# Kernel tuning notes

Measured on AMD Instinct MI355X. Metric: run time of the kernel, lower is better.

Reference implementation:

```python
import jax, jax.numpy as jnp
import numpy as np

WS = 7           # window_size
NUM_HEADS = 4
DIM = 128
BNW = 4096       # batch * num_windows
NW = 64          # windows per image (attn_mask leading dim)
N = WS * WS      # tokens per window = 49


def make_rel_idx(ws: int) -> np.ndarray:
    coords = np.stack(np.meshgrid(np.arange(ws), np.arange(ws), indexing='ij'))  # (2, ws, ws)
    flat = coords.reshape(2, -1)                                                  # (2, N)
    rel = flat[:, :, None] - flat[:, None, :]                                     # (2, N, N)
    rel = rel.transpose(1, 2, 0).copy()
    rel[:, :, 0] += ws - 1
    rel[:, :, 1] += ws - 1
    rel[:, :, 0] *= 2 * ws - 1
    return rel.sum(-1).astype(np.int32)                                           # (N, N)


def setup_inputs() -> dict:
    key = jax.random.key(0)
    ks = jax.random.split(key, 4)
    x = jax.random.normal(ks[0], (BNW, N, DIM), dtype=jnp.float32)
    attn_mask = jnp.zeros((NW, N, N), dtype=jnp.float32)
    qkv_w = jax.random.normal(ks[1], (3 * DIM, DIM), dtype=jnp.float32) * 0.02
    qkv_b = jnp.zeros((3 * DIM,), dtype=jnp.float32)
    proj_w = jax.random.normal(ks[2], (DIM, DIM), dtype=jnp.float32) * 0.02
    proj_b = jnp.zeros((DIM,), dtype=jnp.float32)
    bias_table = jax.random.normal(ks[3], ((2 * WS - 1) ** 2, NUM_HEADS), dtype=jnp.float32) * 0.02
    rel_idx = jnp.asarray(make_rel_idx(WS))
    return {"x": x, "attn_mask": attn_mask, "qkv_w": qkv_w, "qkv_b": qkv_b,
            "proj_w": proj_w, "proj_b": proj_b, "bias_table": bias_table,
            "rel_idx": rel_idx}


def reference(x, attn_mask, qkv_w, qkv_b, proj_w, proj_b, bias_table, rel_idx):
    BnW, n, C = x.shape
    H = NUM_HEADS
    hd = C // H
    scale = hd ** -0.5
    # qkv projection: (BnW, n, 3C) -> (3, BnW, H, n, hd)
    qkv = (x @ qkv_w.T + qkv_b).reshape(BnW, n, 3, H, hd).transpose(2, 0, 3, 1, 4)
    q, k, v = qkv[0], qkv[1], qkv[2]
    attn = jnp.einsum('bhnd,bhmd->bhnm', q * scale, k)          # (BnW, H, n, n)
    bias = bias_table[rel_idx]                                   # (n, n, H)
    attn = attn + bias.transpose(2, 0, 1)[None]                  # broadcast (1, H, n, n)
    nW = attn_mask.shape[0]
    attn = attn.reshape(-1, nW, H, n, n) + attn_mask[None, :, None]
    attn = attn.reshape(-1, H, n, n)
    attn = jax.nn.softmax(attn, axis=-1)
    out = jnp.einsum('bhnm,bhmd->bhnd', attn, v)                 # (BnW, H, n, hd)
    out = out.transpose(0, 2, 1, 3).reshape(BnW, n, C)
    return out @ proj_w.T + proj_b
```

## Files before the change

### kernel.cpp

```cpp
#include <hip/hip_runtime.h>

#define NT   49
#define HD   32
#define NH   4
#define DIM  128
#define SCALEQ 0.17677669529663687f

typedef __attribute__((ext_vector_type(8))) short short8;
typedef __attribute__((ext_vector_type(4))) short short4v;
typedef __attribute__((ext_vector_type(4))) float floatx4;
typedef short8 short8a __attribute__((may_alias));
typedef short4v short4a __attribute__((may_alias));
typedef unsigned long long ulla __attribute__((may_alias));
typedef unsigned long long ull;

__device__ __forceinline__ short f2b(float f) {
    union { float f; unsigned u; } v; v.f = f;
    return (short)((v.u + 0x7fffu + ((v.u >> 16) & 1u)) >> 16);
}
__device__ __forceinline__ float b2f(short s) {
    union { unsigned u; float f; } v; v.u = ((unsigned)(unsigned short)s) << 16;
    return v.f;
}

#if __has_builtin(__builtin_amdgcn_mfma_f32_16x16x16bf16_1k)
__device__ __forceinline__ floatx4 MFMA16(short4v a, short4v b, floatx4 c) {
    return __builtin_amdgcn_mfma_f32_16x16x16bf16_1k(a, b, c, 0, 0, 0);
}
#else
__device__ __forceinline__ floatx4 MFMA16(short4v a, short4v b, floatx4 c) {
    short8 a8 = {a[0], a[1], a[2], a[3], 0, 0, 0, 0};
    short8 b8 = {b[0], b[1], b[2], b[3], 0, 0, 0, 0};
    return __builtin_amdgcn_mfma_f32_16x16x32_bf16(a8, b8, c, 0, 0, 0);
}
#endif

__global__ __launch_bounds__(256) void wmsa_prep(
        const float* __restrict__ qkvw, const float* __restrict__ projw,
        const float* __restrict__ btab, const int* __restrict__ ridx,
        const float* __restrict__ mask,
        short* __restrict__ wqkv, short* __restrict__ wproj,
        short* __restrict__ cmb) {
    __shared__ __align__(16) int   s_ridx[NT * NT];
    __shared__ __align__(16) float s_btab[169 * 4];
    __shared__ __align__(16) float s_mask[NT * NT];

    const int wdw = blockIdx.x;
    const int tid = threadIdx.x;

    {
        int g = wdw * 256 + tid;
        const float* src = (g < 12288) ? (qkvw + g * 4) : (projw + (g - 12288) * 4);
        float4 v = *(const float4*)src;
        float s = (g < 4096) ? SCALEQ : 1.0f;
        ull pk =  (ull)(unsigned short)f2b(v.x * s)
                | ((ull)(unsigned short)f2b(v.y * s) << 16)
                | ((ull)(unsigned short)f2b(v.z * s) << 32)
                | ((ull)(unsigned short)f2b(v.w * s) << 48);
        if (g < 12288) *(ulla*)(wqkv + g * 4) = pk;
        else           *(ulla*)(wproj + (g - 12288) * 4) = pk;
    }

    for (int i = tid; i < NT * NT; i += 256) s_ridx[i] = ridx[i];
    for (int i = tid; i < 169 * 4; i += 256) s_btab[i] = btab[i];
    {
        const float* mw = mask + (size_t)wdw * NT * NT;
        for (int i = tid; i < NT * NT; i += 256) s_mask[i] = mw[i];
    }
    __syncthreads();

    #pragma unroll
    for (int gi = 0; gi < 4; ++gi) {
        int g = gi * 256 + tid;
        int cc = g & 15, qq = (g >> 4) & 3, tile = g >> 6;
        int it = tile >> 2, jt = tile & 3;
        int col = jt * 16 + cc;
        int rowb = it * 16 + qq * 4;
        if (col >= NT) {
            ull m16 = (unsigned short)f2b(-1e30f);
            ull pk = m16 | (m16 << 16) | (m16 << 32) | (m16 << 48);
            #pragma unroll
            for (int h = 0; h < NH; ++h)
                *(ulla*)(cmb + (((size_t)wdw * NH + h) << 12) + g * 4) = pk;
        } else {
            float bt[4][4], mv[4];
            #pragma unroll
            for (int r = 0; r < 4; ++r) {
                int row = rowb + r;
                if (row >= NT) {
                    bt[r][0] = bt[r][1] = bt[r][2] = bt[r][3] = 0.f;
                    mv[r] = 0.f;
                } else {
                    int ri = s_ridx[row * NT + col];
                    float4 b4 = *(const float4*)(s_btab + ri * 4);
                    bt[r][0] = b4.x; bt[r][1] = b4.y; bt[r][2] = b4.z; bt[r][3] = b4.w;
                    mv[r] = s_mask[row * NT + col];
                }
            }
            #pragma unroll
            for (int h = 0; h < NH; ++h) {
                ull pk =  (ull)(unsigned short)f2b(bt[0][h] + mv[0])
                        | ((ull)(unsigned short)f2b(bt[1][h] + mv[1]) << 16)
                        | ((ull)(unsigned short)f2b(bt[2][h] + mv[2]) << 32)
                        | ((ull)(unsigned short)f2b(bt[3][h] + mv[3]) << 48);
                *(ulla*)(cmb + (((size_t)wdw * NH + h) << 12) + g * 4) = pk;
            }
        }
    }
}

#define RWAVE 8192
#define OSTR  136
#define LDSB  32768

__global__ __launch_bounds__(256, 4) void wmsa_main(
    const float* __restrict__ x,
    const float* __restrict__ qkvb, const float* __restrict__ projb,
    const short* __restrict__ wqkv, const short* __restrict__ wproj,
    const short* __restrict__ cmb, float* __restrict__ out)
{
    __shared__ __align__(16) char pool[LDSB];
    short* lds = (short*)pool;

    const int b    = blockIdx.x;
    const int wdw  = b & 63;
    const int tid  = threadIdx.x;
    const int wave = tid >> 6;
    const int lane = tid & 63;
    const int qq   = lane >> 4;
    const int cc   = lane & 15;
    const int ccl  = cc & 7, cch = cc >> 3, cm3 = cc & 3;

    const int colbase = wave * 32 + cc;
    float biasv[6];
    #pragma unroll
    for (int j = 0; j < 6; ++j)
        biasv[j] = qkvb[(j >> 1) * DIM + colbase + (j & 1) * 16];

    {
        const float* xb = x + (size_t)b * NT * DIM;
        for (int i = tid; i < NT * 32; i += 256) {
            int t = i >> 5, c4 = (i & 31) << 2;
            float4 v = *(const float4*)(xb + t * DIM + c4);
            ull pk =  (ull)(unsigned short)f2b(v.x)
                    | ((ull)(unsigned short)f2b(v.y) << 16)
                    | ((ull)(unsigned short)f2b(v.z) << 32)
                    | ((ull)(unsigned short)f2b(v.w) << 48);
            *(ulla*)(lds + t * 136 + c4) = pk;
        }
        for (int i = tid; i < (64 - NT) * 32; i += 256) {
            int t = NT + (i >> 5), c4 = (i & 31) << 2;
            *(ulla*)(lds + t * 136 + c4) = 0ull;
        }
    }
    __syncthreads();

    short8 af[4][4];
    #pragma unroll
    for (int it = 0; it < 4; ++it)
        #pragma unroll
        for (int ks = 0; ks < 4; ++ks)
            af[it][ks] = *(const short8a*)(lds + (it * 16 + cc) * 136 + ks * 32 + qq * 8);
    __syncthreads();

    short* qw = (short*)(pool + wave * RWAVE);
    short* kw = qw + 2048;
    short* pw = qw;

    short4v vq[2][4];

    #pragma unroll
    for (int jt6 = 0; jt6 < 6; ++jt6) {
        const int sec = jt6 >> 1, hlf = jt6 & 1;
        short8 bfc[4];
        {
            const int cn = sec * DIM + colbase + hlf * 16;
            #pragma unroll
            for (int ks = 0; ks < 4; ++ks)
                bfc[ks] = *(const short8a*)(wqkv + cn * DIM + ks * 32 + qq * 8);
        }
        float bias = biasv[jt6];
        if (sec == 0) bias *= SCALEQ;
        const floatx4 cinit = {bias, bias, bias, bias};
        #pragma unroll
        for (int it = 0; it < 4; ++it) {
            floatx4 acc = cinit;
            #pragma unroll
            for (int ks = 0; ks < 4; ++ks)
                acc = __builtin_amdgcn_mfma_f32_16x16x32_bf16(af[it][ks], bfc[ks], acc, 0, 0, 0);
            if (sec == 2) {
                short4v pv;
                pv[0] = f2b(acc[0]); pv[1] = f2b(acc[1]);
                pv[2] = f2b(acc[2]); pv[3] = f2b(acc[3]);
                vq[hlf][it] = pv;
            } else {
                short* dst = (sec == 0) ? qw : kw;
                int gb = hlf * 2 + cch;
                #pragma unroll
                for (int r = 0; r < 4; ++r) {
                    int t = it * 16 + qq * 4 + r;
                    dst[t * 32 + ((gb ^ r) << 3) + ccl] = f2b(acc[r]);
                }
            }
        }
    }

    short4v cm[16];
    {
        const short* cw = cmb + (((size_t)wdw * NH + wave) << 12);
        #pragma unroll
        for (int t16 = 0; t16 < 16; ++t16)
            cm[t16] = *(const short4a*)(cw + t16 * 256 + qq * 64 + cc * 4);
    }
    __asm__ volatile("" ::: "memory");

    {
        short8 qf[4], kf[4];
        #pragma unroll
        for (int t = 0; t < 4; ++t) {
            qf[t] = *(const short8a*)(qw + (t * 16 + cc) * 32 + ((qq ^ cm3) << 3));
            kf[t] = *(const short8a*)(kw + (t * 16 + cc) * 32 + ((qq ^ cm3) << 3));
        }
        #pragma unroll
        for (int it = 0; it < 4; ++it) {
            floatx4 s[4];
            #pragma unroll
            for (int jt = 0; jt < 4; ++jt) {
                short4v cb = cm[it * 4 + jt];
                floatx4 ci = {b2f(cb.x), b2f(cb.y), b2f(cb.z), b2f(cb.w)};
                s[jt] = __builtin_amdgcn_mfma_f32_16x16x32_bf16(qf[it], kf[jt], ci, 0, 0, 0);
            }
            #pragma unroll
            for (int r = 0; r < 4; ++r) {
                int t = it * 16 + qq * 4 + r;
                #pragma unroll
                for (int jt = 0; jt < 4; ++jt) {
                    float ee = __expf(s[jt][r]);
                    int g = (jt * 2 + cch) ^ r ^ ((qq & 1) << 2);
                    pw[t * 64 + (g << 3) + ccl] = f2b(ee);
                }
            }
        }
    }
    __asm__ volatile("" ::: "memory");

    floatx4 o[4][2], ssum[4];
    #pragma unroll
    for (int it = 0; it < 4; ++it) {
        o[it][0] = (floatx4){0.f, 0.f, 0.f, 0.f};
        o[it][1] = (floatx4){0.f, 0.f, 0.f, 0.f};
        ssum[it] = (floatx4){0.f, 0.f, 0.f, 0.f};
    }
    const short BONE = (short)0x3F80;
    const short4v ones4 = {BONE, BONE, BONE, BONE};
    #pragma unroll
    for (int rt = 0; rt < 4; ++rt) {
        #pragma unroll
        for (int kt = 0; kt < 4; ++kt) {
            int g = (kt * 2 + (qq >> 1)) ^ cm3 ^ (((cc >> 2) & 1) << 2);
            short4v pf = *(const short4a*)(pw + (rt * 16 + cc) * 64 + (g << 3) + (qq & 1) * 4);
            o[rt][0] = MFMA16(pf, vq[0][kt], o[rt][0]);
            o[rt][1] = MFMA16(pf, vq[1][kt], o[rt][1]);
            ssum[rt] = MFMA16(pf, ones4, ssum[rt]);
        }
    }
    #pragma unroll
    for (int it = 0; it < 4; ++it)
        #pragma unroll
        for (int r = 0; r < 4; ++r) {
            float inv = 1.0f / ssum[it][r];
            o[it][0][r] *= inv;
            o[it][1][r] *= inv;
        }

    short8 pcur[4], pnxt[4];
    float pbv[8];
    #pragma unroll
    for (int ks = 0; ks < 4; ++ks) {
        pcur[ks] = *(const short8a*)(wproj + cc * DIM + ks * 32 + qq * 8);
        pnxt[ks] = *(const short8a*)(wproj + (16 + cc) * DIM + ks * 32 + qq * 8);
    }
    #pragma unroll
    for (int j = 0; j < 8; ++j) pbv[j] = projb[j * 16 + cc];

    __syncthreads();

    short* ow = (short*)pool;
    #pragma unroll
    for (int it = 0; it < 4; ++it)
        #pragma unroll
        for (int jv = 0; jv < 2; ++jv)
            #pragma unroll
            for (int r = 0; r < 4; ++r) {
                int t = it * 16 + qq * 4 + r;
                ow[t * OSTR + wave * 32 + jv * 16 + cc] = f2b(o[it][jv][r]);
            }
    __syncthreads();

    {
        short8 a2[4];
        #pragma unroll
        for (int ks = 0; ks < 4; ++ks)
            a2[ks] = *(const short8a*)(ow + (wave * 16 + cc) * OSTR + ks * 32 + qq * 8);
        float* outb = out + (size_t)b * NT * DIM;
        #pragma unroll
        for (int jt = 0; jt < 8; ++jt) {
            short8 pfut[4];
            if (jt < 6) {
                int cn = (jt + 2) * 16 + cc;
                #pragma unroll
                for (int ks = 0; ks < 4; ++ks)
                    pfut[ks] = *(const short8a*)(wproj + cn * DIM + ks * 32 + qq * 8);
            }
            float pb = pbv[jt];
            floatx4 acc = {pb, pb, pb, pb};
            #pragma unroll
            for (int ks = 0; ks < 4; ++ks)
                acc = __builtin_amdgcn_mfma_f32_16x16x32_bf16(a2[ks], pcur[ks], acc, 0, 0, 0);
            int col = jt * 16 + cc;
            #pragma unroll
            for (int r = 0; r < 4; ++r) {
                int row = wave * 16 + qq * 4 + r;
                if (row < NT) outb[row * DIM + col] = acc[r];
            }
            #pragma unroll
            for (int ks = 0; ks < 4; ++ks) { pcur[ks] = pnxt[ks]; pnxt[ks] = pfut[ks]; }
        }
    }
}

extern "C" void kernel_launch(void* const* d_in, const int* in_sizes, int n_in,
                              void* d_out, int out_size, void* d_ws, size_t ws_size,
                              hipStream_t stream) {
    const float* x     = (const float*)d_in[0];
    const float* mask  = (const float*)d_in[1];
    const float* qkvw  = (const float*)d_in[2];
    const float* qkvb  = (const float*)d_in[3];
    const float* projw = (const float*)d_in[4];
    const float* projb = (const float*)d_in[5];
    const float* btab  = (const float*)d_in[6];
    const int*   ridx  = (const int*)d_in[7];
    float* outp = (float*)d_out;

    short* wqkv  = (short*)d_ws;
    short* wproj = (short*)((char*)d_ws + 98304);
    short* cmb   = (short*)((char*)d_ws + 131072);

    wmsa_prep<<<64, 256, 0, stream>>>(qkvw, projw, btab, ridx, mask, wqkv, wproj, cmb);
    wmsa_main<<<4096, 256, 0, stream>>>(x, qkvb, projb, wqkv, wproj, cmb, outp);
}
```

Before: 295.7 us.

## Keep Q/K in registers via transposed MFMA, drop LDS round-trip

The Q and K projections are now computed transposed (weights as the A operand), so their bf16 results land directly in the register layout that the QK^T MFMA needs. This removes the scattered LDS stores and reloads of Q and K. The PV stage is also transposed so each lane holds a whole row sum and can write packed 64-bit output stores to LDS instead of scalar stores. The cost is higher register pressure, and the QK^T step now uses two K=16 MFMAs per tile instead of one K=32.

```diff
diff --git a/kernel.cpp b/kernel.cpp
--- a/kernel.cpp
+++ b/kernel.cpp
@@ -132,10 +132,16 @@
     const int ccl  = cc & 7, cch = cc >> 3, cm3 = cc & 3;
 
     const int colbase = wave * 32 + cc;
-    float biasv[6];
-    #pragma unroll
-    for (int j = 0; j < 6; ++j)
-        biasv[j] = qkvb[(j >> 1) * DIM + colbase + (j & 1) * 16];
+    float4 bq[2], bk[2];
+    #pragma unroll
+    for (int hlf = 0; hlf < 2; ++hlf) {
+        bq[hlf] = *(const float4*)(qkvb + 0 * DIM + wave * 32 + hlf * 16 + qq * 4);
+        bk[hlf] = *(const float4*)(qkvb + 1 * DIM + wave * 32 + hlf * 16 + qq * 4);
+        bq[hlf].x *= SCALEQ; bq[hlf].y *= SCALEQ; bq[hlf].z *= SCALEQ; bq[hlf].w *= SCALEQ;
+    }
+    float bv[2];
+    bv[0] = qkvb[2 * DIM + colbase];
+    bv[1] = qkvb[2 * DIM + colbase + 16];
 
     {
         const float* xb = x + (size_t)b * NT * DIM;
@@ -163,11 +169,9 @@
             af[it][ks] = *(const short8a*)(lds + (it * 16 + cc) * 136 + ks * 32 + qq * 8);
     __syncthreads();
 
-    short* qw = (short*)(pool + wave * RWAVE);
-    short* kw = qw + 2048;
-    short* pw = qw;
-
-    short4v vq[2][4];
+    short* pw = (short*)(pool + wave * RWAVE);
+
+    short4v qt[2][4], kt[2][4], vq[2][4];
 
     #pragma unroll
     for (int jt6 = 0; jt6 < 6; ++jt6) {
@@ -179,28 +183,32 @@
             for (int ks = 0; ks < 4; ++ks)
                 bfc[ks] = *(const short8a*)(wqkv + cn * DIM + ks * 32 + qq * 8);
         }
-        float bias = biasv[jt6];
-        if (sec == 0) bias *= SCALEQ;
-        const floatx4 cinit = {bias, bias, bias, bias};
-        #pragma unroll
-        for (int it = 0; it < 4; ++it) {
-            floatx4 acc = cinit;
-            #pragma unroll
-            for (int ks = 0; ks < 4; ++ks)
-                acc = __builtin_amdgcn_mfma_f32_16x16x32_bf16(af[it][ks], bfc[ks], acc, 0, 0, 0);
-            if (sec == 2) {
-                short4v pv;
-                pv[0] = f2b(acc[0]); pv[1] = f2b(acc[1]);
-                pv[2] = f2b(acc[2]); pv[3] = f2b(acc[3]);
-                vq[hlf][it] = pv;
-            } else {
-                short* dst = (sec == 0) ? qw : kw;
-                int gb = hlf * 2 + cch;
+        if (sec < 2) {
+            float4 b4 = (sec == 0) ? bq[hlf] : bk[hlf];
+            const floatx4 cinit = {b4.x, b4.y, b4.z, b4.w};
+            #pragma unroll
+            for (int tt = 0; tt < 4; ++tt) {
+                floatx4 acc = cinit;
                 #pragma unroll
-                for (int r = 0; r < 4; ++r) {
-                    int t = it * 16 + qq * 4 + r;
-                    dst[t * 32 + ((gb ^ r) << 3) + ccl] = f2b(acc[r]);
-                }
+                for (int ks = 0; ks < 4; ++ks)
+                    acc = __builtin_amdgcn_mfma_f32_16x16x32_bf16(bfc[ks], af[tt][ks], acc, 0, 0, 0);
+                short4v f;
+                f[0] = f2b(acc[0]); f[1] = f2b(acc[1]);
+                f[2] = f2b(acc[2]); f[3] = f2b(acc[3]);
+                if (sec == 0) qt[hlf][tt] = f; else kt[hlf][tt] = f;
+            }
+        } else {
+            const floatx4 cinit = {bv[hlf], bv[hlf], bv[hlf], bv[hlf]};
+            #pragma unroll
+            for (int it = 0; it < 4; ++it) {
+                floatx4 acc = cinit;
+                #pragma unroll
+                for (int ks = 0; ks < 4; ++ks)
+                    acc = __builtin_amdgcn_mfma_f32_16x16x32_bf16(af[it][ks], bfc[ks], acc, 0, 0, 0);
+                short4v f;
+                f[0] = f2b(acc[0]); f[1] = f2b(acc[1]);
+                f[2] = f2b(acc[2]); f[3] = f2b(acc[3]);
+                vq[hlf][it] = f;
             }
         }
     }
@@ -212,66 +220,53 @@
         for (int t16 = 0; t16 < 16; ++t16)
             cm[t16] = *(const short4a*)(cw + t16 * 256 + qq * 64 + cc * 4);
     }
+
+    #pragma unroll
+    for (int it = 0; it < 4; ++it) {
+        floatx4 s[4];
+        #pragma unroll
+        for (int jt = 0; jt < 4; ++jt) {
+            short4v cb = cm[it * 4 + jt];
+            floatx4 ci = {b2f(cb.x), b2f(cb.y), b2f(cb.z), b2f(cb.w)};
+            ci = MFMA16(qt[0][it], kt[0][jt], ci);
+            s[jt] = MFMA16(qt[1][it], kt[1][jt], ci);
+        }
+        #pragma unroll
+        for (int r = 0; r < 4; ++r) {
+            int t = it * 16 + qq * 4 + r;
+            #pragma unroll
+            for (int jt = 0; jt < 4; ++jt) {
+                float ee = __expf(s[jt][r]);
+                int g = (jt * 2 + cch) ^ r ^ ((qq & 1) << 2);
+                pw[t * 64 + (g << 3) + ccl] = f2b(ee);
+            }
+        }
+    }
     __asm__ volatile("" ::: "memory");
 
-    {
-        short8 qf[4], kf[4];
-        #pragma unroll
-        for (int t = 0; t < 4; ++t) {
-            qf[t] = *(const short8a*)(qw + (t * 16 + cc) * 32 + ((qq ^ cm3) << 3));
-            kf[t] = *(const short8a*)(kw + (t * 16 + cc) * 32 + ((qq ^ cm3) << 3));
-        }
-        #pragma unroll
-        for (int it = 0; it < 4; ++it) {
-            floatx4 s[4];
-            #pragma unroll
-            for (int jt = 0; jt < 4; ++jt) {
-                short4v cb = cm[it * 4 + jt];
-                floatx4 ci = {b2f(cb.x), b2f(cb.y), b2f(cb.z), b2f(cb.w)};
-                s[jt] = __builtin_amdgcn_mfma_f32_16x16x32_bf16(qf[it], kf[jt], ci, 0, 0, 0);
-            }
-            #pragma unroll
-            for (int r = 0; r < 4; ++r) {
-                int t = it * 16 + qq * 4 + r;
-                #pragma unroll
-                for (int jt = 0; jt < 4; ++jt) {
-                    float ee = __expf(s[jt][r]);
-                    int g = (jt * 2 + cch) ^ r ^ ((qq & 1) << 2);
-                    pw[t * 64 + (g << 3) + ccl] = f2b(ee);
-                }
-            }
-        }
-    }
-    __asm__ volatile("" ::: "memory");
-
-    floatx4 o[4][2], ssum[4];
-    #pragma unroll
-    for (int it = 0; it < 4; ++it) {
-        o[it][0] = (floatx4){0.f, 0.f, 0.f, 0.f};
-        o[it][1] = (floatx4){0.f, 0.f, 0.f, 0.f};
-        ssum[it] = (floatx4){0.f, 0.f, 0.f, 0.f};
-    }
+    floatx4 o[2][4];
     const short BONE = (short)0x3F80;
     const short4v ones4 = {BONE, BONE, BONE, BONE};
     #pragma unroll
-    for (int rt = 0; rt < 4; ++rt) {
-        #pragma unroll
-        for (int kt = 0; kt < 4; ++kt) {
-            int g = (kt * 2 + (qq >> 1)) ^ cm3 ^ (((cc >> 2) & 1) << 2);
-            short4v pf = *(const short4a*)(pw + (rt * 16 + cc) * 64 + (g << 3) + (qq & 1) * 4);
-            o[rt][0] = MFMA16(pf, vq[0][kt], o[rt][0]);
-            o[rt][1] = MFMA16(pf, vq[1][kt], o[rt][1]);
-            ssum[rt] = MFMA16(pf, ones4, ssum[rt]);
-        }
-    }
-    #pragma unroll
-    for (int it = 0; it < 4; ++it)
-        #pragma unroll
-        for (int r = 0; r < 4; ++r) {
-            float inv = 1.0f / ssum[it][r];
-            o[it][0][r] *= inv;
-            o[it][1][r] *= inv;
-        }
+    for (int tt = 0; tt < 4; ++tt) {
+        short4v ptb[4];
+        #pragma unroll
+        for (int kt4 = 0; kt4 < 4; ++kt4) {
+            int g = (kt4 * 2 + (qq >> 1)) ^ cm3 ^ (((cc >> 2) & 1) << 2);
+            ptb[kt4] = *(const short4a*)(pw + (tt * 16 + cc) * 64 + (g << 3) + (qq & 1) * 4);
+        }
+        floatx4 a0 = {0.f, 0.f, 0.f, 0.f}, a1 = a0, sm = a0;
+        #pragma unroll
+        for (int kt4 = 0; kt4 < 4; ++kt4) {
+            a0 = MFMA16(vq[0][kt4], ptb[kt4], a0);
+            a1 = MFMA16(vq[1][kt4], ptb[kt4], a1);
+            sm = MFMA16(ones4, ptb[kt4], sm);
+        }
+        float inv = 1.0f / sm[0];
+        #pragma unroll
+        for (int r = 0; r < 4; ++r) { a0[r] *= inv; a1[r] *= inv; }
+        o[0][tt] = a0; o[1][tt] = a1;
+    }
 
     short8 pcur[4], pnxt[4];
     float pbv[8];
@@ -287,14 +282,17 @@
 
     short* ow = (short*)pool;
     #pragma unroll
-    for (int it = 0; it < 4; ++it)
-        #pragma unroll
-        for (int jv = 0; jv < 2; ++jv)
-            #pragma unroll
-            for (int r = 0; r < 4; ++r) {
-                int t = it * 16 + qq * 4 + r;
-                ow[t * OSTR + wave * 32 + jv * 16 + cc] = f2b(o[it][jv][r]);
-            }
+    for (int hlf = 0; hlf < 2; ++hlf)
+        #pragma unroll
+        for (int tt = 0; tt < 4; ++tt) {
+            int t  = tt * 16 + cc;
+            int f0 = wave * 32 + hlf * 16 + qq * 4;
+            ull pk =  (ull)(unsigned short)f2b(o[hlf][tt][0])
+                    | ((ull)(unsigned short)f2b(o[hlf][tt][1]) << 16)
+                    | ((ull)(unsigned short)f2b(o[hlf][tt][2]) << 32)
+                    | ((ull)(unsigned short)f2b(o[hlf][tt][3]) << 48);
+            *(ulla*)(ow + t * OSTR + f0) = pk;
+        }
     __syncthreads();
 
     {
```

Result: slower. 308.0 us (+4.2%).
